# Kernel optimization log

Measured on AMD Instinct MI355X. Metric: run time of the kernel, lower is better.

## Reference

```python
import jax, jax.numpy as jnp
import numpy as np

N_NODES = 50000
N_EDGES = 800000
D_IN = 128
D_OUT = 128


def setup_inputs() -> dict:
    key = jax.random.key(0)
    k1, k2, k3, k4 = jax.random.split(key, 4)
    feature = jax.random.normal(k1, (N_NODES, D_IN), dtype=jnp.float32)
    edge_src = jax.random.randint(k2, (N_EDGES,), 0, N_NODES, dtype=jnp.int32)
    edge_dst = jax.random.randint(k3, (N_EDGES,), 0, N_NODES, dtype=jnp.int32)
    W = jax.random.normal(k4, (D_IN, D_OUT), dtype=jnp.float32) * (1.0 / np.sqrt(D_IN))
    b = jnp.zeros((D_OUT,), dtype=jnp.float32)
    return {"feature": feature, "edge_src": edge_src, "edge_dst": edge_dst, "W": W, "b": b}


def reference(feature, edge_src, edge_dst, W, b):
    # copy_src + sum reduce: for each edge, copy src node feature, sum into dst node
    msgs = feature[edge_src]  # [E, D_IN] gather
    h = jax.ops.segment_sum(msgs, edge_dst, num_segments=N_NODES)  # [N, D_IN]
    # linear + activation (relu)
    return jax.nn.relu(h @ W + b)
```

## Files before the change

### kernel.cpp

```cpp
#include <hip/hip_runtime.h>
#include <hip/hip_fp16.h>


constexpr int N    = 50000;
constexpr int E    = 800000;
constexpr int D    = 128;
constexpr int CAP  = 64;
constexpr int NT   = 3125;
constexpr int ZSTR = 136;
constexpr int NR   = 782;
constexpr int HB   = 500;
constexpr int EPB  = E / HB;

using f16x8 = __attribute__((ext_vector_type(8))) _Float16;
using f32x4 = __attribute__((ext_vector_type(4))) float;

__global__ void setup(const float* __restrict__ W, _Float16* __restrict__ Wf,
                      _Float16* __restrict__ Z) {
    if (blockIdx.x == 8) {
        if (threadIdx.x < D) Z[(size_t)N * D + threadIdx.x] = (_Float16)0.f;
        return;
    }
    int t = blockIdx.x * 256 + threadIdx.x;
    int ct = t >> 8, ks = (t >> 6) & 3, lane = t & 63;
    int q = lane >> 4, li = lane & 15;
    _Float16 v[8];
    #pragma unroll
    for (int j = 0; j < 8; ++j)
        v[j] = (_Float16)W[(ks * 32 + q * 8 + j) * D + ct * 16 + li];
    *(f16x8*)(Wf + (size_t)t * 8) = *(const f16x8*)v;
}

__global__ __launch_bounds__(256) void midk(
        const float* __restrict__ feature,
        const int*   __restrict__ edst,
        const _Float16* __restrict__ Wf,
        int* __restrict__ hist,
        _Float16* __restrict__ Z) {
    __shared__ int h[NR];
    __shared__ _Float16 zs[4][16 * ZSTR];
    const int tid = threadIdx.x;

    if (blockIdx.x < HB) {
        const int b = blockIdx.x;
        for (int i = tid; i < NR; i += 256) h[i] = 0;
        __syncthreads();
        const int e0 = b * EPB;
        for (int i = tid; i < EPB; i += 256)
            atomicAdd(&h[edst[e0 + i] >> 6], 1);
        __syncthreads();
        for (int i = tid; i < NR; i += 256) hist[b * NR + i] = h[i];
        return;
    }

    const int wave = tid >> 6, lane = tid & 63;
    const int wt = (blockIdx.x - HB) * 4 + wave;
    if (wt >= NT) return;
    const int q = lane >> 4, li = lane & 15;

    const float* fp = feature + (size_t)(wt * 16 + li) * D + q * 8;
    f16x8 afr[4];
    #pragma unroll
    for (int ks = 0; ks < 4; ++ks) {
        const float4 u0 = *(const float4*)(fp + ks * 32);
        const float4 u1 = *(const float4*)(fp + ks * 32 + 4);
        afr[ks][0] = (_Float16)u0.x; afr[ks][1] = (_Float16)u0.y;
        afr[ks][2] = (_Float16)u0.z; afr[ks][3] = (_Float16)u0.w;
        afr[ks][4] = (_Float16)u1.x; afr[ks][5] = (_Float16)u1.y;
        afr[ks][6] = (_Float16)u1.z; afr[ks][7] = (_Float16)u1.w;
    }

    f32x4 acc[8];
    #pragma unroll
    for (int ct = 0; ct < 8; ++ct) acc[ct] = (f32x4){0.f, 0.f, 0.f, 0.f};
    #pragma unroll
    for (int ks = 0; ks < 4; ++ks)
        #pragma unroll
        for (int ct = 0; ct < 8; ++ct) {
            const f16x8 b = *(const f16x8*)(Wf + (size_t)((ct * 4 + ks) * 64 + lane) * 8);
            acc[ct] = __builtin_amdgcn_mfma_f32_16x16x32_f16(afr[ks], b, acc[ct], 0, 0, 0);
        }

    _Float16* zt = zs[wave];
    #pragma unroll
    for (int ct = 0; ct < 8; ++ct)
        #pragma unroll
        for (int r = 0; r < 4; ++r)
            zt[(q * 4 + r) * ZSTR + ct * 16 + li] = (_Float16)acc[ct][r];
    #pragma unroll
    for (int it = 0; it < 4; ++it) {
        const f16x8 v = *(const f16x8*)(zt + (it * 4 + q) * ZSTR + li * 8);
        *(f16x8*)(Z + (size_t)(wt * 16 + it * 4 + q) * D + li * 8) = v;
    }
}

__global__ void scank(int* __restrict__ hist, int* __restrict__ total) {
    const int r    = blockIdx.x;
    const int lane = threadIdx.x;
    int h[8], sum = 0;
    #pragma unroll
    for (int j = 0; j < 8; ++j) {
        const int idx = lane * 8 + j;
        h[j] = (idx < HB) ? hist[idx * NR + r] : 0;
        sum += h[j];
    }
    int incl = sum;
    #pragma unroll
    for (int off = 1; off < 64; off <<= 1) {
        int u = __shfl_up(incl, off);
        if (lane >= off) incl += u;
    }
    int run = incl - sum;
    #pragma unroll
    for (int j = 0; j < 8; ++j) {
        const int idx = lane * 8 + j;
        if (idx < HB) hist[idx * NR + r] = run;
        run += h[j];
    }
    if (lane == 63) total[r] = run;
}

__global__ __launch_bounds__(256) void partk(
        const int* __restrict__ esrc,
        const int* __restrict__ edst,
        const int* __restrict__ blockBase,
        const int* __restrict__ total,
        int* __restrict__ rangeStartG,
        unsigned int* __restrict__ part) {
    __shared__ int rs[NR];
    __shared__ int mb[NR];
    __shared__ int rk[NR];
    const int tid = threadIdx.x;
    const int b   = blockIdx.x;

    if (tid < 64) {
        int carry = 0;
        #pragma unroll
        for (int c = 0; c < 13; ++c) {
            const int idx = c * 64 + tid;
            const int v = (idx < NR) ? total[idx] : 0;
            int incl = v;
            #pragma unroll
            for (int off = 1; off < 64; off <<= 1) {
                int u = __shfl_up(incl, off);
                if (tid >= off) incl += u;
            }
            if (idx < NR) rs[idx] = incl - v + carry;
            carry += __shfl(incl, 63);
        }
    }
    for (int i = tid; i < NR; i += 256) { mb[i] = blockBase[b * NR + i]; rk[i] = 0; }
    __syncthreads();
    if (b == 0)
        for (int i = tid; i < NR; i += 256) rangeStartG[i] = rs[i];

    const int e0 = b * EPB;
    for (int i = tid; i < EPB; i += 256) {
        const int s = esrc[e0 + i];
        const int d = edst[e0 + i];
        const int r = d >> 6;
        const int k = atomicAdd(&rk[r], 1);
        part[rs[r] + mb[r] + k] = ((unsigned)(d & 63) << 16) | (unsigned)s;
    }
}

__global__ __launch_bounds__(256, 4) void csrgather(
        const unsigned int* __restrict__ part,
        const int* __restrict__ rangeStart,
        const int* __restrict__ total,
        const _Float16* __restrict__ Z,
        const float* __restrict__ bias,
        float* __restrict__ out) {
    __shared__ unsigned short bkt[32 * CAP];
    __shared__ int deg[32];
    __shared__ unsigned char perm[32];
    const int r   = blockIdx.x >> 1;
    const int sub = blockIdx.x & 1;
    const int tid = threadIdx.x;

    if (tid < 32) deg[tid] = 0;
    __syncthreads();
    const int rsv = rangeStart[r], tot = total[r];
    for (int i = tid; i < tot; i += 256) {
        const unsigned p = part[rsv + i];
        const int local = p >> 16;
        if ((local >> 5) == sub) {
            const int l5 = local & 31;
            const int k = atomicAdd(&deg[l5], 1);
            if (k < CAP) bkt[l5 * CAP + k] = (unsigned short)(p & 0xFFFF);
        }
    }
    __syncthreads();

    if (tid < 32) {
        const int d = deg[tid];
        int rk = 0;
        for (int j = 0; j < 32; ++j) {
            const int dj = deg[j];
            rk += (dj > d) || (dj == d && j < tid);
        }
        perm[rk] = (unsigned char)tid;
    }
    __syncthreads();

    const int wave = tid >> 6, lane = tid & 63;
    const int g = lane >> 4, li = lane & 15;

    #pragma unroll 1
    for (int grp = 0; grp < 2; ++grp) {
        const int l0 = perm[wave * 8 + grp * 4 + 0];
        const int l1 = perm[wave * 8 + grp * 4 + 1];
        const int l2 = perm[wave * 8 + grp * 4 + 2];
        const int l3 = perm[wave * 8 + grp * 4 + 3];
        const int d0 = min(deg[l0], CAP), d1 = min(deg[l1], CAP);
        const int d2 = min(deg[l2], CAP), d3 = min(deg[l3], CAP);

        float a0[8] = {0,0,0,0,0,0,0,0};
        float a1[8] = {0,0,0,0,0,0,0,0};
        float a2[8] = {0,0,0,0,0,0,0,0};
        float a3[8] = {0,0,0,0,0,0,0,0};

        const int mx = max(max(d0, d1), max(d2, d3));
        #pragma unroll 1
        for (int base = 0; base < mx; base += 16) {
            f16x8 h0[4], h1[4], h2[4], h3[4];
            #pragma unroll
            for (int t = 0; t < 4; ++t) {
                const int rr = base + t * 4 + g;
                int s0 = bkt[l0 * CAP + rr];
                int s1 = bkt[l1 * CAP + rr];
                int s2 = bkt[l2 * CAP + rr];
                int s3 = bkt[l3 * CAP + rr];
                s0 = (rr < d0) ? s0 : N;
                s1 = (rr < d1) ? s1 : N;
                s2 = (rr < d2) ? s2 : N;
                s3 = (rr < d3) ? s3 : N;
                h0[t] = *(const f16x8*)(Z + (size_t)s0 * D + li * 8);
                h1[t] = *(const f16x8*)(Z + (size_t)s1 * D + li * 8);
                h2[t] = *(const f16x8*)(Z + (size_t)s2 * D + li * 8);
                h3[t] = *(const f16x8*)(Z + (size_t)s3 * D + li * 8);
            }
            #pragma unroll
            for (int t = 0; t < 4; ++t)
                #pragma unroll
                for (int j = 0; j < 8; ++j) {
                    a0[j] += (float)h0[t][j];
                    a1[j] += (float)h1[t][j];
                    a2[j] += (float)h2[t][j];
                    a3[j] += (float)h3[t][j];
                }
        }

        #pragma unroll
        for (int j = 0; j < 8; ++j) {
            a0[j] += __shfl_xor(a0[j], 16); a0[j] += __shfl_xor(a0[j], 32);
            a1[j] += __shfl_xor(a1[j], 16); a1[j] += __shfl_xor(a1[j], 32);
            a2[j] += __shfl_xor(a2[j], 16); a2[j] += __shfl_xor(a2[j], 32);
            a3[j] += __shfl_xor(a3[j], 16); a3[j] += __shfl_xor(a3[j], 32);
        }

        const int ln = (g == 0) ? l0 : (g == 1) ? l1 : (g == 2) ? l2 : l3;
        float av[8];
        #pragma unroll
        for (int j = 0; j < 8; ++j)
            av[j] = (g == 0) ? a0[j] : (g == 1) ? a1[j] : (g == 2) ? a2[j] : a3[j];

        const int node = (r << 6) + (sub << 5) + ln;
        if (node < N) {
            const float4 b0 = *(const float4*)(bias + li * 8);
            const float4 b1 = *(const float4*)(bias + li * 8 + 4);
            float4 o0, o1;
            o0.x = fmaxf(av[0] + b0.x, 0.f); o0.y = fmaxf(av[1] + b0.y, 0.f);
            o0.z = fmaxf(av[2] + b0.z, 0.f); o0.w = fmaxf(av[3] + b0.w, 0.f);
            o1.x = fmaxf(av[4] + b1.x, 0.f); o1.y = fmaxf(av[5] + b1.y, 0.f);
            o1.z = fmaxf(av[6] + b1.z, 0.f); o1.w = fmaxf(av[7] + b1.w, 0.f);
            float* op = out + (size_t)node * D + li * 8;
            *(float4*)op       = o0;
            *(float4*)(op + 4) = o1;
        }
    }
}

extern "C" void kernel_launch(void* const* d_in, const int* in_sizes, int n_in,
                              void* d_out, int out_size, void* d_ws, size_t ws_size,
                              hipStream_t stream) {
    const float* feature = (const float*)d_in[0];
    const int*   esrc    = (const int*)d_in[1];
    const int*   edst    = (const int*)d_in[2];
    const float* W       = (const float*)d_in[3];
    const float* bias    = (const float*)d_in[4];
    float*       out     = (float*)d_out;

    _Float16*     Z      = (_Float16*)d_ws;
    _Float16*     Wf     = Z + (size_t)(N + 1) * D;
    int*          hist   = (int*)(Wf + 16384);
    int*          total  = hist + HB * NR;
    int*          rangeS = total + NR;
    unsigned int* part   = (unsigned int*)(rangeS + NR);

    setup<<<9, 256, 0, stream>>>(W, Wf, Z);
    midk <<<HB + (NT + 3) / 4, 256, 0, stream>>>(feature, edst, Wf, hist, Z);
    scank<<<NR, 64, 0, stream>>>(hist, total);
    partk<<<HB, 256, 0, stream>>>(esrc, edst, hist, total, rangeS, part);
    csrgather<<<NR * 2, 256, 0, stream>>>(part, rangeS, total, Z, bias, out);
}
```

Before: 145.6 us.

## Replace histogram/scan/partition CSR build with direct per-node bucket fill via global atomics

Removes the two-pass counting sort (per-block histograms, scan kernel, partition kernel) and fills a fixed-capacity per-destination bucket directly, using global atomicAdd on a per-node counter inside the fused projection kernel. The gather kernel then loads its 32 nodes' buckets with one coalesced load instead of rescanning a partitioned range. This cuts two kernel launches and several passes over the edge list, at the cost of 800k contended global atomics and scattered 2-byte stores. Waves also pair their heaviest and lightest node groups for load balance, and the bias load is hoisted.

```diff
diff --git a/kernel.cpp b/kernel.cpp
--- a/kernel.cpp
+++ b/kernel.cpp
@@ -8,17 +8,23 @@
 constexpr int CAP  = 64;
 constexpr int NT   = 3125;
 constexpr int ZSTR = 136;
-constexpr int NR   = 782;
-constexpr int HB   = 500;
-constexpr int EPB  = E / HB;
+constexpr int BB   = 128;
+constexpr int EPB  = E / BB;
+constexpr int NCNT = 50016;
+constexpr int GB   = 1563;
 
 using f16x8 = __attribute__((ext_vector_type(8))) _Float16;
 using f32x4 = __attribute__((ext_vector_type(4))) float;
 
 __global__ void setup(const float* __restrict__ W, _Float16* __restrict__ Wf,
-                      _Float16* __restrict__ Z) {
+                      _Float16* __restrict__ Z, int* __restrict__ cnt) {
     if (blockIdx.x == 8) {
         if (threadIdx.x < D) Z[(size_t)N * D + threadIdx.x] = (_Float16)0.f;
+        return;
+    }
+    if (blockIdx.x >= 9) {
+        const int i0 = (blockIdx.x - 9) * 256 + threadIdx.x;
+        for (int i = i0; i < NCNT; i += 64 * 256) cnt[i] = 0;
         return;
     }
     int t = blockIdx.x * 256 + threadIdx.x;
@@ -33,28 +39,28 @@
 
 __global__ __launch_bounds__(256) void midk(
         const float* __restrict__ feature,
+        const int*   __restrict__ esrc,
         const int*   __restrict__ edst,
         const _Float16* __restrict__ Wf,
-        int* __restrict__ hist,
+        int* __restrict__ cnt,
+        unsigned short* __restrict__ bucket,
         _Float16* __restrict__ Z) {
-    __shared__ int h[NR];
+    const int tid = threadIdx.x;
+
+    if (blockIdx.x < BB) {
+        const int e0 = blockIdx.x * EPB;
+        for (int i = tid; i < EPB; i += 256) {
+            const int s = esrc[e0 + i];
+            const int d = edst[e0 + i];
+            const int k = atomicAdd(&cnt[d], 1);
+            if (k < CAP) bucket[(size_t)d * CAP + k] = (unsigned short)s;
+        }
+        return;
+    }
+
     __shared__ _Float16 zs[4][16 * ZSTR];
-    const int tid = threadIdx.x;
-
-    if (blockIdx.x < HB) {
-        const int b = blockIdx.x;
-        for (int i = tid; i < NR; i += 256) h[i] = 0;
-        __syncthreads();
-        const int e0 = b * EPB;
-        for (int i = tid; i < EPB; i += 256)
-            atomicAdd(&h[edst[e0 + i] >> 6], 1);
-        __syncthreads();
-        for (int i = tid; i < NR; i += 256) hist[b * NR + i] = h[i];
-        return;
-    }
-
     const int wave = tid >> 6, lane = tid & 63;
-    const int wt = (blockIdx.x - HB) * 4 + wave;
+    const int wt = (blockIdx.x - BB) * 4 + wave;
     if (wt >= NT) return;
     const int q = lane >> 4, li = lane & 15;
 
@@ -94,101 +100,22 @@
     }
 }
 
-__global__ void scank(int* __restrict__ hist, int* __restrict__ total) {
-    const int r    = blockIdx.x;
-    const int lane = threadIdx.x;
-    int h[8], sum = 0;
-    #pragma unroll
-    for (int j = 0; j < 8; ++j) {
-        const int idx = lane * 8 + j;
-        h[j] = (idx < HB) ? hist[idx * NR + r] : 0;
-        sum += h[j];
-    }
-    int incl = sum;
-    #pragma unroll
-    for (int off = 1; off < 64; off <<= 1) {
-        int u = __shfl_up(incl, off);
-        if (lane >= off) incl += u;
-    }
-    int run = incl - sum;
-    #pragma unroll
-    for (int j = 0; j < 8; ++j) {
-        const int idx = lane * 8 + j;
-        if (idx < HB) hist[idx * NR + r] = run;
-        run += h[j];
-    }
-    if (lane == 63) total[r] = run;
-}
-
-__global__ __launch_bounds__(256) void partk(
-        const int* __restrict__ esrc,
-        const int* __restrict__ edst,
-        const int* __restrict__ blockBase,
-        const int* __restrict__ total,
-        int* __restrict__ rangeStartG,
-        unsigned int* __restrict__ part) {
-    __shared__ int rs[NR];
-    __shared__ int mb[NR];
-    __shared__ int rk[NR];
-    const int tid = threadIdx.x;
-    const int b   = blockIdx.x;
-
-    if (tid < 64) {
-        int carry = 0;
-        #pragma unroll
-        for (int c = 0; c < 13; ++c) {
-            const int idx = c * 64 + tid;
-            const int v = (idx < NR) ? total[idx] : 0;
-            int incl = v;
-            #pragma unroll
-            for (int off = 1; off < 64; off <<= 1) {
-                int u = __shfl_up(incl, off);
-                if (tid >= off) incl += u;
-            }
-            if (idx < NR) rs[idx] = incl - v + carry;
-            carry += __shfl(incl, 63);
-        }
-    }
-    for (int i = tid; i < NR; i += 256) { mb[i] = blockBase[b * NR + i]; rk[i] = 0; }
-    __syncthreads();
-    if (b == 0)
-        for (int i = tid; i < NR; i += 256) rangeStartG[i] = rs[i];
-
-    const int e0 = b * EPB;
-    for (int i = tid; i < EPB; i += 256) {
-        const int s = esrc[e0 + i];
-        const int d = edst[e0 + i];
-        const int r = d >> 6;
-        const int k = atomicAdd(&rk[r], 1);
-        part[rs[r] + mb[r] + k] = ((unsigned)(d & 63) << 16) | (unsigned)s;
-    }
-}
-
-__global__ __launch_bounds__(256, 4) void csrgather(
-        const unsigned int* __restrict__ part,
-        const int* __restrict__ rangeStart,
-        const int* __restrict__ total,
+__global__ __launch_bounds__(256) void csrgather(
+        const int* __restrict__ cnt,
+        const unsigned short* __restrict__ bucket,
         const _Float16* __restrict__ Z,
         const float* __restrict__ bias,
         float* __restrict__ out) {
     __shared__ unsigned short bkt[32 * CAP];
     __shared__ int deg[32];
     __shared__ unsigned char perm[32];
-    const int r   = blockIdx.x >> 1;
-    const int sub = blockIdx.x & 1;
     const int tid = threadIdx.x;
-
-    if (tid < 32) deg[tid] = 0;
-    __syncthreads();
-    const int rsv = rangeStart[r], tot = total[r];
-    for (int i = tid; i < tot; i += 256) {
-        const unsigned p = part[rsv + i];
-        const int local = p >> 16;
-        if ((local >> 5) == sub) {
-            const int l5 = local & 31;
-            const int k = atomicAdd(&deg[l5], 1);
-            if (k < CAP) bkt[l5 * CAP + k] = (unsigned short)(p & 0xFFFF);
-        }
+    const int n0  = blockIdx.x * 32;
+
+    ((uint4*)bkt)[tid] = ((const uint4*)(bucket + (size_t)n0 * CAP))[tid];
+    if (tid < 32) {
+        const int n = n0 + tid;
+        deg[tid] = (n < N) ? min(cnt[n], CAP) : 0;
     }
     __syncthreads();
 
@@ -205,15 +132,18 @@
 
     const int wave = tid >> 6, lane = tid & 63;
     const int g = lane >> 4, li = lane & 15;
+    const float4 b0 = *(const float4*)(bias + li * 8);
+    const float4 b1 = *(const float4*)(bias + li * 8 + 4);
 
     #pragma unroll 1
-    for (int grp = 0; grp < 2; ++grp) {
-        const int l0 = perm[wave * 8 + grp * 4 + 0];
-        const int l1 = perm[wave * 8 + grp * 4 + 1];
-        const int l2 = perm[wave * 8 + grp * 4 + 2];
-        const int l3 = perm[wave * 8 + grp * 4 + 3];
-        const int d0 = min(deg[l0], CAP), d1 = min(deg[l1], CAP);
-        const int d2 = min(deg[l2], CAP), d3 = min(deg[l3], CAP);
+    for (int gsel = 0; gsel < 2; ++gsel) {
+        const int gi = gsel ? (7 - wave) : wave;
+        const int l0 = perm[gi * 4 + 0];
+        const int l1 = perm[gi * 4 + 1];
+        const int l2 = perm[gi * 4 + 2];
+        const int l3 = perm[gi * 4 + 3];
+        const int d0 = deg[l0], d1 = deg[l1];
+        const int d2 = deg[l2], d3 = deg[l3];
 
         float a0[8] = {0,0,0,0,0,0,0,0};
         float a1[8] = {0,0,0,0,0,0,0,0};
@@ -265,10 +195,8 @@
         for (int j = 0; j < 8; ++j)
             av[j] = (g == 0) ? a0[j] : (g == 1) ? a1[j] : (g == 2) ? a2[j] : a3[j];
 
-        const int node = (r << 6) + (sub << 5) + ln;
+        const int node = n0 + ln;
         if (node < N) {
-            const float4 b0 = *(const float4*)(bias + li * 8);
-            const float4 b1 = *(const float4*)(bias + li * 8 + 4);
             float4 o0, o1;
             o0.x = fmaxf(av[0] + b0.x, 0.f); o0.y = fmaxf(av[1] + b0.y, 0.f);
             o0.z = fmaxf(av[2] + b0.z, 0.f); o0.w = fmaxf(av[3] + b0.w, 0.f);
@@ -291,16 +219,12 @@
     const float* bias    = (const float*)d_in[4];
     float*       out     = (float*)d_out;
 
-    _Float16*     Z      = (_Float16*)d_ws;
-    _Float16*     Wf     = Z + (size_t)(N + 1) * D;
-    int*          hist   = (int*)(Wf + 16384);
-    int*          total  = hist + HB * NR;
-    int*          rangeS = total + NR;
-    unsigned int* part   = (unsigned int*)(rangeS + NR);
-
-    setup<<<9, 256, 0, stream>>>(W, Wf, Z);
-    midk <<<HB + (NT + 3) / 4, 256, 0, stream>>>(feature, edst, Wf, hist, Z);
-    scank<<<NR, 64, 0, stream>>>(hist, total);
-    partk<<<HB, 256, 0, stream>>>(esrc, edst, hist, total, rangeS, part);
-    csrgather<<<NR * 2, 256, 0, stream>>>(part, rangeS, total, Z, bias, out);
-}
+    _Float16*       Z      = (_Float16*)d_ws;
+    _Float16*       Wf     = Z + (size_t)(N + 1) * D;
+    int*            cnt    = (int*)(Wf + 16384);
+    unsigned short* bucket = (unsigned short*)(cnt + NCNT);
+
+    setup<<<73, 256, 0, stream>>>(W, Wf, Z, cnt);
+    midk <<<BB + (NT + 3) / 4, 256, 0, stream>>>(feature, esrc, edst, Wf, cnt, bucket, Z);
+    csrgather<<<GB, 256, 0, stream>>>(cnt, bucket, Z, bias, out);
+}
```

After: 155.3 us. 1.07x slower.

## Process full 64-node range per csrgather block with balanced group assignment

Applied to the files above, without the earlier changes.

csrgather now handles all 64 destination nodes of a range in one block instead of splitting each range across two blocks. This halves the redundant scans of the partition list, which were filtered by sub-range. Each wave takes four groups of four nodes in a snake order over the degree-sorted permutation, to balance work across waves. The midk kernel is reordered so GEMM blocks come first and histogram blocks last, and the bias loads are hoisted out of the loop. The trade-off is fewer, longer blocks and the removed occupancy hint in the launch bounds.

```diff
diff --git a/kernel.cpp b/kernel.cpp
--- a/kernel.cpp
+++ b/kernel.cpp
@@ -7,6 +7,7 @@
 constexpr int D    = 128;
 constexpr int CAP  = 64;
 constexpr int NT   = 3125;
+constexpr int TB   = 782;
 constexpr int ZSTR = 136;
 constexpr int NR   = 782;
 constexpr int HB   = 500;
@@ -41,8 +42,8 @@
     __shared__ _Float16 zs[4][16 * ZSTR];
     const int tid = threadIdx.x;
 
-    if (blockIdx.x < HB) {
-        const int b = blockIdx.x;
+    if (blockIdx.x >= TB) {
+        const int b = blockIdx.x - TB;
         for (int i = tid; i < NR; i += 256) h[i] = 0;
         __syncthreads();
         const int e0 = b * EPB;
@@ -54,7 +55,7 @@
     }
 
     const int wave = tid >> 6, lane = tid & 63;
-    const int wt = (blockIdx.x - HB) * 4 + wave;
+    const int wt = blockIdx.x * 4 + wave;
     if (wt >= NT) return;
     const int q = lane >> 4, li = lane & 15;
 
@@ -164,39 +165,36 @@
     }
 }
 
-__global__ __launch_bounds__(256, 4) void csrgather(
+__global__ __launch_bounds__(256) void csrgather(
         const unsigned int* __restrict__ part,
         const int* __restrict__ rangeStart,
         const int* __restrict__ total,
         const _Float16* __restrict__ Z,
         const float* __restrict__ bias,
         float* __restrict__ out) {
-    __shared__ unsigned short bkt[32 * CAP];
-    __shared__ int deg[32];
-    __shared__ unsigned char perm[32];
-    const int r   = blockIdx.x >> 1;
-    const int sub = blockIdx.x & 1;
+    __shared__ unsigned short bkt[64 * CAP];
+    __shared__ int deg[64];
+    __shared__ unsigned char perm[64];
+    const int r   = blockIdx.x;
     const int tid = threadIdx.x;
 
-    if (tid < 32) deg[tid] = 0;
+    if (tid < 64) deg[tid] = 0;
     __syncthreads();
+
     const int rsv = rangeStart[r], tot = total[r];
     for (int i = tid; i < tot; i += 256) {
         const unsigned p = part[rsv + i];
         const int local = p >> 16;
-        if ((local >> 5) == sub) {
-            const int l5 = local & 31;
-            const int k = atomicAdd(&deg[l5], 1);
-            if (k < CAP) bkt[l5 * CAP + k] = (unsigned short)(p & 0xFFFF);
-        }
+        const int k = atomicAdd(&deg[local], 1);
+        if (k < CAP) bkt[local * CAP + k] = (unsigned short)(p & 0xFFFF);
     }
     __syncthreads();
 
-    if (tid < 32) {
-        const int d = deg[tid];
+    if (tid < 64) {
+        const int d = min(deg[tid], CAP);
         int rk = 0;
-        for (int j = 0; j < 32; ++j) {
-            const int dj = deg[j];
+        for (int j = 0; j < 64; ++j) {
+            const int dj = min(deg[j], CAP);
             rk += (dj > d) || (dj == d && j < tid);
         }
         perm[rk] = (unsigned char)tid;
@@ -205,13 +203,19 @@
 
     const int wave = tid >> 6, lane = tid & 63;
     const int g = lane >> 4, li = lane & 15;
+    const float4 b0 = *(const float4*)(bias + li * 8);
+    const float4 b1 = *(const float4*)(bias + li * 8 + 4);
 
     #pragma unroll 1
-    for (int grp = 0; grp < 2; ++grp) {
-        const int l0 = perm[wave * 8 + grp * 4 + 0];
-        const int l1 = perm[wave * 8 + grp * 4 + 1];
-        const int l2 = perm[wave * 8 + grp * 4 + 2];
-        const int l3 = perm[wave * 8 + grp * 4 + 3];
+    for (int gsel = 0; gsel < 4; ++gsel) {
+        const int gi = (gsel == 0) ? wave
+                     : (gsel == 1) ? (7 - wave)
+                     : (gsel == 2) ? (8 + wave)
+                                   : (15 - wave);
+        const int l0 = perm[gi * 4 + 0];
+        const int l1 = perm[gi * 4 + 1];
+        const int l2 = perm[gi * 4 + 2];
+        const int l3 = perm[gi * 4 + 3];
         const int d0 = min(deg[l0], CAP), d1 = min(deg[l1], CAP);
         const int d2 = min(deg[l2], CAP), d3 = min(deg[l3], CAP);
 
@@ -265,10 +269,8 @@
         for (int j = 0; j < 8; ++j)
             av[j] = (g == 0) ? a0[j] : (g == 1) ? a1[j] : (g == 2) ? a2[j] : a3[j];
 
-        const int node = (r << 6) + (sub << 5) + ln;
+        const int node = (r << 6) + ln;
         if (node < N) {
-            const float4 b0 = *(const float4*)(bias + li * 8);
-            const float4 b1 = *(const float4*)(bias + li * 8 + 4);
             float4 o0, o1;
             o0.x = fmaxf(av[0] + b0.x, 0.f); o0.y = fmaxf(av[1] + b0.y, 0.f);
             o0.z = fmaxf(av[2] + b0.z, 0.f); o0.w = fmaxf(av[3] + b0.w, 0.f);
@@ -299,8 +301,8 @@
     unsigned int* part   = (unsigned int*)(rangeS + NR);
 
     setup<<<9, 256, 0, stream>>>(W, Wf, Z);
-    midk <<<HB + (NT + 3) / 4, 256, 0, stream>>>(feature, edst, Wf, hist, Z);
+    midk <<<TB + HB, 256, 0, stream>>>(feature, edst, Wf, hist, Z);
     scank<<<NR, 64, 0, stream>>>(hist, total);
     partk<<<HB, 256, 0, stream>>>(esrc, edst, hist, total, rangeS, part);
-    csrgather<<<NR * 2, 256, 0, stream>>>(part, rangeS, total, Z, bias, out);
-}
+    csrgather<<<NR, 256, 0, stream>>>(part, rangeS, total, Z, bias, out);
+}
```

After: 150.5 us. 1.03x slower.
